# Optimization experiments

Measured on AMD Instinct MI355X. Metric: run time of the kernel, lower is better.

Reference implementation:

```python
import jax, jax.numpy as jnp
import numpy as np
import math

HIDDEN = 1024
HEADS = 16
HEAD_DIM = HIDDEN // HEADS
TEMP_K = 1000.0  # custom temperature multiplier applied after masking
B, S = 2, 2048


def setup_inputs() -> dict:
    key = jax.random.key(0)
    ks = jax.random.split(key, 4)
    scale = 1.0 / math.sqrt(HIDDEN)
    return {
        "x": jax.random.normal(ks[0], (B, S, HIDDEN), dtype=jnp.float32),
        "W_qkv": jax.random.normal(ks[1], (HIDDEN, 3 * HIDDEN), dtype=jnp.float32) * scale,
        "b_qkv": jnp.zeros((3 * HIDDEN,), dtype=jnp.float32),
        "W_out": jax.random.normal(ks[2], (HIDDEN, HIDDEN), dtype=jnp.float32) * scale,
        "b_out": jnp.zeros((HIDDEN,), dtype=jnp.float32),
    }


def reference(x, W_qkv, b_qkv, W_out, b_out):
    b, s, _ = x.shape
    qkv = x @ W_qkv + b_qkv                                    # [b,s,3*hidden]
    qkv = qkv.reshape(b, s, 3, HEADS, HEAD_DIM)
    qkv = jnp.transpose(qkv, (2, 0, 3, 1, 4))                  # [3,b,h,s,d]
    q, k, v = qkv[0], qkv[1], qkv[2]
    scores = jnp.einsum('bhqd,bhkd->bhqk', q, k) / math.sqrt(HEAD_DIM)
    causal = jnp.tril(jnp.ones((s, s), dtype=bool))            # [s,s]
    scores = jnp.where(causal[None, None], scores, -jnp.inf)
    probs = jax.nn.softmax(scores * TEMP_K, axis=-1)           # temp-scaled softmax
    attn = jnp.einsum('bhqk,bhkd->bhqd', probs, v)             # [b,h,s,d]
    attn = jnp.transpose(attn, (0, 2, 1, 3)).reshape(b, s, HIDDEN)
    return attn @ W_out + b_out
```

## Files before the change

### kernel.cpp

```cpp
#include <hip/hip_runtime.h>
#include <hip/hip_bf16.h>

#define BATCH 2
#define SEQ 2048
#define HID 1024
#define NHEAD 16
#define HDIM 64
#define L2SCALE 180.3368800721f
#define NEGBIG (-1.0e30f)

typedef __bf16 bf16;
typedef __bf16 bf16x4 __attribute__((ext_vector_type(4)));
typedef __bf16 bf16x8 __attribute__((ext_vector_type(8)));
typedef float f32x16 __attribute__((ext_vector_type(16)));

union BQ  { bf16x4 v; unsigned u[2]; };
union BF8 { bf16x8 v; unsigned u[4]; };

__device__ __constant__ int TAB_QT[30]  = {5,6,7,8,9,10,11,11,12,12,13,13,14,14,15,15, 4,10, 3,9,15, 2,8,14, 1,7,13, 0,6,12};
__device__ __constant__ int TAB_K0[30]  = {0,0,0,0,0,0,0,12,0,12,0,12,0,12,0,12, 0,12, 0,12,24, 0,12,24, 0,12,24, 0,12,24};
__device__ __constant__ int TAB_NIT[30] = {12,12,12,12,12,12,12,12,12,12,12,12,12,12,12,12, 10,10, 8,8,8, 6,6,6, 4,4,4, 2,2,2};
__device__ __constant__ int TAB_PID[30] = {-1,0,2,4,6,8,10,11,12,13,15,16,18,19,21,22, -1,9, -1,7,23, -1,5,20, -1,3,17, -1,1,14};

__global__ __launch_bounds__(256) void transpose_split_kernel(
    const float* __restrict__ W, bf16* __restrict__ Thi, bf16* __restrict__ Tlo,
    int K, int N)
{
    __shared__ float T[64][65];
    const int tid = threadIdx.x;
    const int kBase = blockIdx.y * 64;
    const int nBase = blockIdx.x * 64;
    {
        const int k0 = tid >> 4;
        const int nc = (tid & 15) * 4;
#pragma unroll
        for (int kk = 0; kk < 4; kk++) {
            int k = k0 + kk * 16;
            float4 v = *(const float4*)(W + (size_t)(kBase + k) * N + nBase + nc);
            T[k][nc] = v.x; T[k][nc + 1] = v.y; T[k][nc + 2] = v.z; T[k][nc + 3] = v.w;
        }
    }
    __syncthreads();
    {
        const int n = tid >> 2;
        const int kc = (tid & 3) * 16;
        bf16x8 h0, h1, l0, l1;
#pragma unroll
        for (int j = 0; j < 8; j++) {
            float a = T[kc + j][n];
            float c = T[kc + 8 + j][n];
            bf16 ha = (bf16)a, hc = (bf16)c;
            h0[j] = ha; h1[j] = hc;
            l0[j] = (bf16)(a - (float)ha);
            l1[j] = (bf16)(c - (float)hc);
        }
        size_t dst = (size_t)(nBase + n) * K + kBase + kc;
        *(bf16x8*)(Thi + dst)     = h0;
        *(bf16x8*)(Thi + dst + 8) = h1;
        if (Tlo) {
            *(bf16x8*)(Tlo + dst)     = l0;
            *(bf16x8*)(Tlo + dst + 8) = l1;
        }
    }
}

__global__ __launch_bounds__(256) void xsplit_kernel(
    const float* __restrict__ X, bf16* __restrict__ Xhi, bf16* __restrict__ Xlo)
{
    const int i = blockIdx.x * 256 + threadIdx.x;
    float4 v = ((const float4*)X)[i];
    float xs[4] = {v.x, v.y, v.z, v.w};
    bf16x4 h, l;
#pragma unroll
    for (int j = 0; j < 4; j++) {
        h[j] = (bf16)xs[j];
        l[j] = (bf16)(xs[j] - (float)h[j]);
    }
    ((bf16x4*)Xhi)[i] = h;
    ((bf16x4*)Xlo)[i] = l;
}

__global__ __launch_bounds__(256) void vtrans_kernel(
    const bf16* __restrict__ vv, bf16* __restrict__ vtr)
{
    __shared__ bf16 T[64][72];
    const int tid = threadIdx.x;
    const int bh = blockIdx.y;
    const int st = blockIdx.x;
    const int r  = tid >> 2;
    const int c0 = (tid & 3) * 16;
    const bf16* src = vv + ((size_t)bh * SEQ + st * 64) * HDIM;
    bf16x8 a = *(const bf16x8*)(src + (size_t)r * HDIM + c0);
    bf16x8 b = *(const bf16x8*)(src + (size_t)r * HDIM + c0 + 8);
    *(bf16x8*)&T[r][c0]     = a;
    *(bf16x8*)&T[r][c0 + 8] = b;
    __syncthreads();
    bf16x8 o0, o1;
#pragma unroll
    for (int i = 0; i < 8; i++) {
        o0[i] = T[c0 + i][r];
        o1[i] = T[c0 + 8 + i][r];
    }
    bf16* dst = vtr + ((size_t)bh * HDIM + r) * SEQ + st * 64 + c0;
    *(bf16x8*)(dst)     = o0;
    *(bf16x8*)(dst + 8) = o1;
}

__global__ __launch_bounds__(256) void gemm_qkv_mfma(
    const bf16* __restrict__ Xhi, const bf16* __restrict__ Xlo,
    const bf16* __restrict__ Wthi, const bf16* __restrict__ Wtlo,
    const float* __restrict__ bias,
    bf16* __restrict__ qhi, bf16* __restrict__ qlo,
    bf16* __restrict__ khi, bf16* __restrict__ klo, bf16* __restrict__ vv)
{
    __shared__ __align__(16) bf16 Wh[128][40];
    __shared__ __align__(16) bf16 Wl[128][40];

    const int tid = threadIdx.x;
    const int wave = tid >> 6, lane = tid & 63;
    const int lm = lane & 31, lq2 = lane >> 5;
    const int wave_s = wave & 1, wave_n = wave >> 1;
    const int nBase = blockIdx.x * 128;
    const int sBase = blockIdx.y * 128;
    const bool isV = (nBase >= 2 * HID);

    const int sr = tid >> 1, skc = (tid & 1) * 16;

    f32x16 acc[2][2];
#pragma unroll
    for (int st = 0; st < 2; st++)
#pragma unroll
      for (int nt = 0; nt < 2; nt++)
#pragma unroll
        for (int r = 0; r < 16; r++) acc[st][nt][r] = 0.f;

    const bf16* xph[2];
    const bf16* xpl[2];
#pragma unroll
    for (int st = 0; st < 2; st++) {
        size_t row = (size_t)(sBase + wave_s * 64 + st * 32 + lm);
        xph[st] = Xhi + row * HID + lq2 * 8;
        xpl[st] = Xlo + row * HID + lq2 * 8;
    }
    const bf16* wbh = Wthi + (size_t)(nBase + sr) * HID + skc;
    const bf16* wbl = Wtlo + (size_t)(nBase + sr) * HID + skc;

    bf16x8 cw[2], cwl[2] = {};
    cw[0] = *(const bf16x8*)(wbh);
    cw[1] = *(const bf16x8*)(wbh + 8);
    if (!isV) {
        cwl[0] = *(const bf16x8*)(wbl);
        cwl[1] = *(const bf16x8*)(wbl + 8);
    }

    for (int k0 = 0; k0 < HID; k0 += 32) {
        bf16x8 xh_c[2][2], xl_c[2][2] = {};
#pragma unroll
        for (int st = 0; st < 2; st++)
#pragma unroll
          for (int kh = 0; kh < 2; kh++) {
            xh_c[st][kh] = *(const bf16x8*)(xph[st] + k0 + kh * 16);
            if (!isV) xl_c[st][kh] = *(const bf16x8*)(xpl[st] + k0 + kh * 16);
          }

        __syncthreads();
        *(bf16x8*)&Wh[sr][skc]     = cw[0];
        *(bf16x8*)&Wh[sr][skc + 8] = cw[1];
        if (!isV) {
            *(bf16x8*)&Wl[sr][skc]     = cwl[0];
            *(bf16x8*)&Wl[sr][skc + 8] = cwl[1];
        }
        __syncthreads();

        bf16x8 nw[2] = {}, nwl[2] = {};
        if (k0 + 32 < HID) {
            nw[0] = *(const bf16x8*)(wbh + k0 + 32);
            nw[1] = *(const bf16x8*)(wbh + k0 + 32 + 8);
            if (!isV) {
                nwl[0] = *(const bf16x8*)(wbl + k0 + 32);
                nwl[1] = *(const bf16x8*)(wbl + k0 + 32 + 8);
            }
        }

#pragma unroll
        for (int kh = 0; kh < 2; kh++) {
            const int ko = kh * 16 + lq2 * 8;
            bf16x8 aWh[2], aWl[2];
#pragma unroll
            for (int nt = 0; nt < 2; nt++) {
                aWh[nt] = *(bf16x8*)&Wh[wave_n * 64 + nt * 32 + lm][ko];
                if (!isV) aWl[nt] = *(bf16x8*)&Wl[wave_n * 64 + nt * 32 + lm][ko];
            }
#pragma unroll
            for (int nt = 0; nt < 2; nt++)
#pragma unroll
              for (int st = 0; st < 2; st++) {
                acc[st][nt] = __builtin_amdgcn_mfma_f32_32x32x16_bf16(aWh[nt], xh_c[st][kh], acc[st][nt], 0, 0, 0);
                if (!isV) {
                    acc[st][nt] = __builtin_amdgcn_mfma_f32_32x32x16_bf16(aWh[nt], xl_c[st][kh], acc[st][nt], 0, 0, 0);
                    acc[st][nt] = __builtin_amdgcn_mfma_f32_32x32x16_bf16(aWl[nt], xh_c[st][kh], acc[st][nt], 0, 0, 0);
                }
              }
        }
        cw[0] = nw[0]; cw[1] = nw[1];
        cwl[0] = nwl[0]; cwl[1] = nwl[1];
    }

#pragma unroll
    for (int st = 0; st < 2; st++) {
        int s = sBase + wave_s * 64 + st * 32 + lm;
        int bb = s >> 11, ss = s & 2047;
#pragma unroll
        for (int nt = 0; nt < 2; nt++) {
#pragma unroll
            for (int q4 = 0; q4 < 4; q4++) {
                int n = nBase + wave_n * 64 + nt * 32 + 8 * q4 + 4 * lq2;
                float4 bv = *(const float4*)(bias + n);
                float vals[4];
                vals[0] = acc[st][nt][q4 * 4 + 0] + bv.x;
                vals[1] = acc[st][nt][q4 * 4 + 1] + bv.y;
                vals[2] = acc[st][nt][q4 * 4 + 2] + bv.z;
                vals[3] = acc[st][nt][q4 * 4 + 3] + bv.w;
                int which = n >> 10, h = (n >> 6) & 15, d = n & 63;
                size_t dst = (((size_t)bb * NHEAD + h) * SEQ + ss) * HDIM + d;
                if (which < 2) {
                    bf16x4 hi4, lo4;
#pragma unroll
                    for (int i = 0; i < 4; i++) {
                        hi4[i] = (bf16)vals[i];
                        lo4[i] = (bf16)(vals[i] - (float)hi4[i]);
                    }
                    bf16* ph = (which == 0) ? qhi : khi;
                    bf16* pl = (which == 0) ? qlo : klo;
                    *(bf16x4*)(ph + dst) = hi4;
                    *(bf16x4*)(pl + dst) = lo4;
                } else {
                    bf16x4 v4;
#pragma unroll
                    for (int i = 0; i < 4; i++) v4[i] = (bf16)vals[i];
                    *(bf16x4*)(vv + dst) = v4;
                }
            }
        }
    }
}

__global__ __launch_bounds__(256) void attn_kernel(
    const bf16* __restrict__ Qhi, const bf16* __restrict__ Qlo,
    const bf16* __restrict__ Khg, const bf16* __restrict__ Klg,
    const bf16* __restrict__ Vtr, bf16* __restrict__ attnbuf,
    bf16* __restrict__ PartO, float* __restrict__ Mls)
{
    __shared__ __align__(16) bf16 Khs[64][72];
    __shared__ __align__(16) bf16 Kls[64][72];
    __shared__ __align__(16) bf16 Vt [64][72];

    const int tid  = threadIdx.x;
    const int wave = tid >> 6;
    const int lane = tid & 63;
    const int lm   = lane & 31;
    const int lq2  = lane >> 5;

    const int kr  = tid >> 2;
    const int kd0 = (tid & 3) * 16;

    const int slot = blockIdx.x >> 5;
    const int bh   = blockIdx.x & 31;
    const int qt   = TAB_QT[slot];
    const int kt0  = TAB_K0[slot];
    const int nit  = TAB_NIT[slot];
    const int pid  = TAB_PID[slot];
    const int b = bh >> 4, h = bh & 15;
    const size_t headoff = ((size_t)b * NHEAD + h) * SEQ * HDIM;

    const int ql_loc = wave * 32 + lm;
    const int qg = qt * 128 + ql_loc;
    bf16x8 qh[4], qlr[4];
    {
        const bf16* qph = Qhi + headoff + (size_t)qg * HDIM;
        const bf16* qpl = Qlo + headoff + (size_t)qg * HDIM;
#pragma unroll
        for (int c = 0; c < 4; c++) {
            qh[c]  = *(const bf16x8*)(qph + c * 16 + lq2 * 8);
            qlr[c] = *(const bf16x8*)(qpl + c * 16 + lq2 * 8);
        }
    }

    f32x16 O0, O1;
#pragma unroll
    for (int r = 0; r < 16; r++) { O0[r] = 0.f; O1[r] = 0.f; }
    float m_run = NEGBIG, l_run = 0.f;

    const int wave_qmin = qt * 128 + wave * 32;
    const int ktend = kt0 + nit;

    bf16x8 kc[4], vc[2];
    {
        size_t kg = headoff + (size_t)(kt0 * 64 + kr) * HDIM + kd0;
        kc[0] = *(const bf16x8*)(Khg + kg);
        kc[1] = *(const bf16x8*)(Khg + kg + 8);
        kc[2] = *(const bf16x8*)(Klg + kg);
        kc[3] = *(const bf16x8*)(Klg + kg + 8);
        size_t vg = headoff + (size_t)kr * SEQ + kt0 * 64 + kd0;
        vc[0] = *(const bf16x8*)(Vtr + vg);
        vc[1] = *(const bf16x8*)(Vtr + vg + 8);
    }

    for (int kt = kt0; kt < ktend; kt++) {
        __syncthreads();
        *(bf16x8*)&Khs[kr][kd0]     = kc[0];
        *(bf16x8*)&Khs[kr][kd0 + 8] = kc[1];
        *(bf16x8*)&Kls[kr][kd0]     = kc[2];
        *(bf16x8*)&Kls[kr][kd0 + 8] = kc[3];
        *(bf16x8*)&Vt[kr][kd0]      = vc[0];
        *(bf16x8*)&Vt[kr][kd0 + 8]  = vc[1];
        __syncthreads();

        bf16x8 kn[4], vn[2];
        const bool more = (kt + 1 < ktend);
        if (more) {
            size_t kg = headoff + (size_t)((kt + 1) * 64 + kr) * HDIM + kd0;
            kn[0] = *(const bf16x8*)(Khg + kg);
            kn[1] = *(const bf16x8*)(Khg + kg + 8);
            kn[2] = *(const bf16x8*)(Klg + kg);
            kn[3] = *(const bf16x8*)(Klg + kg + 8);
            size_t vg = headoff + (size_t)kr * SEQ + (kt + 1) * 64 + kd0;
            vn[0] = *(const bf16x8*)(Vtr + vg);
            vn[1] = *(const bf16x8*)(Vtr + vg + 8);
        }

        if (kt * 64 <= wave_qmin + 31) {
            f32x16 s[2];
#pragma unroll
            for (int r = 0; r < 16; r++) { s[0][r] = 0.f; s[1][r] = 0.f; }
#pragma unroll
            for (int c = 0; c < 4; c++) {
                bf16x8 ah0 = *(bf16x8*)&Khs[lm][c * 16 + lq2 * 8];
                bf16x8 al0 = *(bf16x8*)&Kls[lm][c * 16 + lq2 * 8];
                bf16x8 ah1 = *(bf16x8*)&Khs[32 + lm][c * 16 + lq2 * 8];
                bf16x8 al1 = *(bf16x8*)&Kls[32 + lm][c * 16 + lq2 * 8];
                s[0] = __builtin_amdgcn_mfma_f32_32x32x16_bf16(ah0, qh[c],  s[0], 0, 0, 0);
                s[0] = __builtin_amdgcn_mfma_f32_32x32x16_bf16(ah0, qlr[c], s[0], 0, 0, 0);
                s[0] = __builtin_amdgcn_mfma_f32_32x32x16_bf16(al0, qh[c],  s[0], 0, 0, 0);
                s[1] = __builtin_amdgcn_mfma_f32_32x32x16_bf16(ah1, qh[c],  s[1], 0, 0, 0);
                s[1] = __builtin_amdgcn_mfma_f32_32x32x16_bf16(ah1, qlr[c], s[1], 0, 0, 0);
                s[1] = __builtin_amdgcn_mfma_f32_32x32x16_bf16(al1, qh[c],  s[1], 0, 0, 0);
            }

            if (kt * 64 + 63 > wave_qmin) {
                const int kbase = kt * 64 + 4 * lq2;
#pragma unroll
                for (int mt = 0; mt < 2; mt++)
#pragma unroll
                  for (int r = 0; r < 16; r++) {
                    int koff = (r & 3) + 8 * (r >> 2) + 32 * mt;
                    float L = s[mt][r] * L2SCALE;
                    if (kbase + koff > qg) L = NEGBIG;
                    s[mt][r] = L;
                  }
            } else {
#pragma unroll
                for (int mt = 0; mt < 2; mt++)
#pragma unroll
                  for (int r = 0; r < 16; r++) s[mt][r] *= L2SCALE;
            }

            float vmax = NEGBIG;
#pragma unroll
            for (int r = 0; r < 16; r++)
                vmax = fmaxf(vmax, fmaxf(s[0][r], s[1][r]));
            vmax = fmaxf(vmax, __shfl_xor(vmax, 32, 64));
            float mnew = fmaxf(m_run, vmax);
            float alpha = exp2f(m_run - mnew);
            float sum = 0.f;
#pragma unroll
            for (int mt = 0; mt < 2; mt++)
#pragma unroll
              for (int r = 0; r < 16; r++) {
                s[mt][r] = exp2f(s[mt][r] - mnew);
                sum += s[mt][r];
              }
            sum += __shfl_xor(sum, 32, 64);
            l_run = l_run * alpha + sum;
            m_run = mnew;
#pragma unroll
            for (int r = 0; r < 16; r++) { O0[r] *= alpha; O1[r] *= alpha; }

            bf16x8 pfrag[4];
#pragma unroll
            for (int mt = 0; mt < 2; mt++)
#pragma unroll
              for (int hh = 0; hh < 2; hh++) {
                BQ A, B;
#pragma unroll
                for (int i = 0; i < 4; i++) {
                    A.v[i] = (bf16)s[mt][8 * hh + i];
                    B.v[i] = (bf16)s[mt][8 * hh + 4 + i];
                }
                unsigned s0_ = lq2 ? A.u[0] : B.u[0];
                unsigned s1_ = lq2 ? A.u[1] : B.u[1];
                unsigned r0 = __shfl_xor(s0_, 32, 64);
                unsigned r1 = __shfl_xor(s1_, 32, 64);
                BF8 f;
                f.u[0] = lq2 ? r0 : A.u[0];
                f.u[1] = lq2 ? r1 : A.u[1];
                f.u[2] = lq2 ? B.u[0] : r0;
                f.u[3] = lq2 ? B.u[1] : r1;
                pfrag[mt * 2 + hh] = f.v;
              }

#pragma unroll
            for (int c = 0; c < 4; c++) {
                bf16x8 va0 = *(bf16x8*)&Vt[lm][c * 16 + lq2 * 8];
                bf16x8 va1 = *(bf16x8*)&Vt[32 + lm][c * 16 + lq2 * 8];
                O0 = __builtin_amdgcn_mfma_f32_32x32x16_bf16(va0, pfrag[c], O0, 0, 0, 0);
                O1 = __builtin_amdgcn_mfma_f32_32x32x16_bf16(va1, pfrag[c], O1, 0, 0, 0);
            }
        }

        if (more) {
#pragma unroll
            for (int i = 0; i < 4; i++) kc[i] = kn[i];
            vc[0] = vn[0]; vc[1] = vn[1];
        }
    }

    if (pid < 0) {
        const float inv = 1.0f / l_run;
        bf16* orow = attnbuf + ((size_t)b * SEQ + qg) * HID + h * HDIM;
#pragma unroll
        for (int g = 0; g < 4; g++) {
            int d0 = 8 * g + 4 * lq2;
            bf16x4 o0, o1;
#pragma unroll
            for (int i = 0; i < 4; i++) {
                o0[i] = (bf16)(O0[4 * g + i] * inv);
                o1[i] = (bf16)(O1[4 * g + i] * inv);
            }
            *(bf16x4*)(orow + d0)      = o0;
            *(bf16x4*)(orow + 32 + d0) = o1;
        }
    } else {
        bf16* prow = PartO + (((size_t)pid * 32 + bh) * 128 + ql_loc) * HDIM;
#pragma unroll
        for (int g = 0; g < 4; g++) {
            int d0 = 8 * g + 4 * lq2;
            bf16x4 o0, o1;
#pragma unroll
            for (int i = 0; i < 4; i++) {
                o0[i] = (bf16)O0[4 * g + i];
                o1[i] = (bf16)O1[4 * g + i];
            }
            *(bf16x4*)(prow + d0)      = o0;
            *(bf16x4*)(prow + 32 + d0) = o1;
        }
        if (lq2 == 0) {
            float2 ml = make_float2(m_run, l_run);
            *(float2*)&Mls[(((size_t)pid * 32 + bh) * 128 + ql_loc) * 2] = ml;
        }
    }
}

__global__ __launch_bounds__(256) void attn_combine(
    const bf16* __restrict__ PartO, const float* __restrict__ Mls,
    bf16* __restrict__ attnbuf)
{
    const int tid = threadIdx.x;
    const int qt = 6 + blockIdx.x / 32;
    const int bh = blockIdx.x & 31;
    const int b = bh >> 4, h = bh & 15;
    const int qrow = tid >> 1;
    const int dh = (tid & 1) * 32;

    int pid0, nch;
    if (qt < 12) { pid0 = 2 * (qt - 6); nch = 2; }
    else         { pid0 = 12 + 3 * (qt - 12); nch = 3; }

    float mv[3], lv[3];
    float M = NEGBIG;
#pragma unroll
    for (int c = 0; c < 3; c++) {
        if (c < nch) {
            float2 ml = *(const float2*)&Mls[(((size_t)(pid0 + c) * 32 + bh) * 128 + qrow) * 2];
            mv[c] = ml.x; lv[c] = ml.y;
            M = fmaxf(M, mv[c]);
        }
    }
    float L = 0.f;
    float acc[32];
#pragma unroll
    for (int i = 0; i < 32; i++) acc[i] = 0.f;
#pragma unroll
    for (int c = 0; c < 3; c++) {
        if (c < nch) {
            float w = exp2f(mv[c] - M);
            L += w * lv[c];
            const bf16* p = PartO + (((size_t)(pid0 + c) * 32 + bh) * 128 + qrow) * HDIM + dh;
#pragma unroll
            for (int g = 0; g < 4; g++) {
                bf16x8 v = *(const bf16x8*)(p + g * 8);
#pragma unroll
                for (int i = 0; i < 8; i++) acc[g * 8 + i] += w * (float)v[i];
            }
        }
    }
    const float inv = 1.0f / L;
    bf16* orow = attnbuf + ((size_t)b * SEQ + qt * 128 + qrow) * HID + h * HDIM + dh;
#pragma unroll
    for (int g = 0; g < 4; g++) {
        bf16x8 o;
#pragma unroll
        for (int i = 0; i < 8; i++) o[i] = (bf16)(acc[g * 8 + i] * inv);
        *(bf16x8*)(orow + g * 8) = o;
    }
}

__global__ __launch_bounds__(256) void gemm_out_mfma(
    const bf16* __restrict__ Attn, const bf16* __restrict__ Wt,
    const float* __restrict__ bias, float* __restrict__ out)
{
    __shared__ __align__(16) bf16 Ah[64][40];

    const int tid = threadIdx.x;
    const int wave = tid >> 6, lane = tid & 63;
    const int lm = lane & 31, lq2 = lane >> 5;
    const int nBase = blockIdx.x * 64;
    const int mBase = blockIdx.y * 128;

    const int ar = tid >> 2, akc = (tid & 3) * 8;
    const bf16* bp    = Attn + (size_t)(mBase + wave * 32 + lm) * HID + lq2 * 8;
    const bf16* abase = Wt + (size_t)(nBase + ar) * HID + akc;

    f32x16 acc[2];
#pragma unroll
    for (int nt = 0; nt < 2; nt++)
#pragma unroll
      for (int r = 0; r < 16; r++) acc[nt][r] = 0.f;

    bf16x8 ca = *(const bf16x8*)(abase);

    for (int k0 = 0; k0 < HID; k0 += 32) {
        bf16x8 cb[2];
        cb[0] = *(const bf16x8*)(bp + k0);
        cb[1] = *(const bf16x8*)(bp + k0 + 16);

        __syncthreads();
        *(bf16x8*)&Ah[ar][akc] = ca;
        __syncthreads();

        bf16x8 na = {};
        if (k0 + 32 < HID) na = *(const bf16x8*)(abase + k0 + 32);

#pragma unroll
        for (int kh = 0; kh < 2; kh++) {
            const int ko = kh * 16 + lq2 * 8;
            bf16x8 aW0 = *(bf16x8*)&Ah[lm][ko];
            bf16x8 aW1 = *(bf16x8*)&Ah[32 + lm][ko];
            acc[0] = __builtin_amdgcn_mfma_f32_32x32x16_bf16(aW0, cb[kh], acc[0], 0, 0, 0);
            acc[1] = __builtin_amdgcn_mfma_f32_32x32x16_bf16(aW1, cb[kh], acc[1], 0, 0, 0);
        }
        ca = na;
    }

    const int m = mBase + wave * 32 + lm;
#pragma unroll
    for (int nt = 0; nt < 2; nt++) {
#pragma unroll
        for (int q4 = 0; q4 < 4; q4++) {
            int n = nBase + nt * 32 + 8 * q4 + 4 * lq2;
            float4 bv = *(const float4*)(bias + n);
            float4 o;
            o.x = acc[nt][q4 * 4 + 0] + bv.x;
            o.y = acc[nt][q4 * 4 + 1] + bv.y;
            o.z = acc[nt][q4 * 4 + 2] + bv.z;
            o.w = acc[nt][q4 * 4 + 3] + bv.w;
            *(float4*)(out + (size_t)m * HID + n) = o;
        }
    }
}

extern "C" void kernel_launch(void* const* d_in, const int* in_sizes, int n_in,
                              void* d_out, int out_size, void* d_ws, size_t ws_size,
                              hipStream_t stream) {
    const float* x    = (const float*)d_in[0];
    const float* Wqkv = (const float*)d_in[1];
    const float* bqkv = (const float*)d_in[2];
    const float* Wout = (const float*)d_in[3];
    const float* bout = (const float*)d_in[4];
    float* out = (float*)d_out;

    const size_t NW  = (size_t)HID * 3 * HID;
    const size_t NWo = (size_t)HID * HID;
    const size_t NT  = (size_t)BATCH * NHEAD * SEQ * HDIM;
    bf16* Wthi = (bf16*)d_ws;
    bf16* Wtlo = Wthi + NW;
    bf16* Wot  = Wtlo + NW;
    bf16* qhi  = Wot + NWo;
    bf16* qlo  = qhi + NT;
    bf16* khi  = qlo + NT;
    bf16* klo  = khi + NT;
    bf16* vv   = klo + NT;
    bf16* attnbuf = vv + NT;
    bf16* Xhi  = attnbuf;
    bf16* Xlo  = attnbuf + NT;
    bf16* vtr  = Xlo;
    bf16* PartO = Wthi;
    float* Mls  = (float*)vv;

    xsplit_kernel<<<dim3((BATCH * SEQ * HID) / 1024), 256, 0, stream>>>(x, Xhi, Xlo);
    transpose_split_kernel<<<dim3(3 * HID / 64, HID / 64), 256, 0, stream>>>(
        Wqkv, Wthi, Wtlo, HID, 3 * HID);
    transpose_split_kernel<<<dim3(HID / 64, HID / 64), 256, 0, stream>>>(
        Wout, Wot, nullptr, HID, HID);
    gemm_qkv_mfma<<<dim3(3 * HID / 128, BATCH * SEQ / 128), 256, 0, stream>>>(
        Xhi, Xlo, Wthi, Wtlo, bqkv, qhi, qlo, khi, klo, vv);
    vtrans_kernel<<<dim3(SEQ / 64, BATCH * NHEAD), 256, 0, stream>>>(vv, vtr);
    attn_kernel<<<dim3(960), 256, 0, stream>>>(
        qhi, qlo, khi, klo, vtr, attnbuf, PartO, Mls);
    attn_combine<<<dim3(320), 256, 0, stream>>>(PartO, Mls, attnbuf);
    gemm_out_mfma<<<dim3(HID / 64, BATCH * SEQ / 128), 256, 0, stream>>>(
        attnbuf, Wot, bout, out);
}
```

Measured before the change: 293.7 us.

## Merge prep kernels, prefetch X tiles in QKV GEMM, enlarge output GEMM tile

Folds the x split and both weight transpose/split kernels into a single prep launch dispatched by block index, which saves two kernel launches. The QKV GEMM now register-prefetches the next X fragments one k-step ahead and changes its shared-memory weight staging layout. The output projection GEMM moves from a 64-wide to a 128x128 tile with a 2x2 wave layout, raising MFMA work per shared-memory load. The cost is higher register pressure and half as many output-GEMM blocks, which may reduce occupancy.

New measurement: 332.0 us. +13.1%, slower.

```diff
diff --git a/kernel.cpp b/kernel.cpp
--- a/kernel.cpp
+++ b/kernel.cpp
@@ -22,14 +22,10 @@
 __device__ __constant__ int TAB_NIT[30] = {12,12,12,12,12,12,12,12,12,12,12,12,12,12,12,12, 10,10, 8,8,8, 6,6,6, 4,4,4, 2,2,2};
 __device__ __constant__ int TAB_PID[30] = {-1,0,2,4,6,8,10,11,12,13,15,16,18,19,21,22, -1,9, -1,7,23, -1,5,20, -1,3,17, -1,1,14};
 
-__global__ __launch_bounds__(256) void transpose_split_kernel(
-    const float* __restrict__ W, bf16* __restrict__ Thi, bf16* __restrict__ Tlo,
-    int K, int N)
+__device__ __forceinline__ void transpose_split_body(
+    float (*T)[65], const float* __restrict__ W, bf16* __restrict__ Thi,
+    bf16* __restrict__ Tlo, int K, int N, int kBase, int nBase, int tid)
 {
-    __shared__ float T[64][65];
-    const int tid = threadIdx.x;
-    const int kBase = blockIdx.y * 64;
-    const int nBase = blockIdx.x * 64;
     {
         const int k0 = tid >> 4;
         const int nc = (tid & 15) * 4;
@@ -64,20 +60,35 @@
     }
 }
 
-__global__ __launch_bounds__(256) void xsplit_kernel(
-    const float* __restrict__ X, bf16* __restrict__ Xhi, bf16* __restrict__ Xlo)
+__global__ __launch_bounds__(256) void prep_kernel(
+    const float* __restrict__ X, bf16* __restrict__ Xhi, bf16* __restrict__ Xlo,
+    const float* __restrict__ Wqkv, bf16* __restrict__ Wthi, bf16* __restrict__ Wtlo,
+    const float* __restrict__ Wout, bf16* __restrict__ Wot)
 {
-    const int i = blockIdx.x * 256 + threadIdx.x;
-    float4 v = ((const float4*)X)[i];
-    float xs[4] = {v.x, v.y, v.z, v.w};
-    bf16x4 h, l;
-#pragma unroll
-    for (int j = 0; j < 4; j++) {
-        h[j] = (bf16)xs[j];
-        l[j] = (bf16)(xs[j] - (float)h[j]);
-    }
-    ((bf16x4*)Xhi)[i] = h;
-    ((bf16x4*)Xlo)[i] = l;
+    __shared__ float T[64][65];
+    const int tid = threadIdx.x;
+    const int bid = blockIdx.x;
+    if (bid < 4096) {
+        const int i = bid * 256 + tid;
+        float4 v = ((const float4*)X)[i];
+        float xs[4] = {v.x, v.y, v.z, v.w};
+        bf16x4 h, l;
+#pragma unroll
+        for (int j = 0; j < 4; j++) {
+            h[j] = (bf16)xs[j];
+            l[j] = (bf16)(xs[j] - (float)h[j]);
+        }
+        ((bf16x4*)Xhi)[i] = h;
+        ((bf16x4*)Xlo)[i] = l;
+    } else if (bid < 4096 + 768) {
+        const int r = bid - 4096;
+        transpose_split_body(T, Wqkv, Wthi, Wtlo, HID, 3 * HID,
+                             (r / 48) * 64, (r % 48) * 64, tid);
+    } else {
+        const int r = bid - 4864;
+        transpose_split_body(T, Wout, Wot, nullptr, HID, HID,
+                             (r / 16) * 64, (r % 16) * 64, tid);
+    }
 }
 
 __global__ __launch_bounds__(256) void vtrans_kernel(
@@ -113,8 +124,8 @@
     bf16* __restrict__ qhi, bf16* __restrict__ qlo,
     bf16* __restrict__ khi, bf16* __restrict__ klo, bf16* __restrict__ vv)
 {
-    __shared__ __align__(16) bf16 Wh[128][40];
-    __shared__ __align__(16) bf16 Wl[128][40];
+    __shared__ __align__(16) bf16 Wh[128][72];
+    __shared__ __align__(16) bf16 Wl[128][72];
 
     const int tid = threadIdx.x;
     const int wave = tid >> 6, lane = tid & 63;
@@ -124,7 +135,8 @@
     const int sBase = blockIdx.y * 128;
     const bool isV = (nBase >= 2 * HID);
 
-    const int sr = tid >> 1, skc = (tid & 1) * 16;
+    const int wr = tid >> 2;
+    const int wc = (tid & 3) * 8;
 
     f32x16 acc[2][2];
 #pragma unroll
@@ -142,43 +154,56 @@
         xph[st] = Xhi + row * HID + lq2 * 8;
         xpl[st] = Xlo + row * HID + lq2 * 8;
     }
-    const bf16* wbh = Wthi + (size_t)(nBase + sr) * HID + skc;
-    const bf16* wbl = Wtlo + (size_t)(nBase + sr) * HID + skc;
+    const bf16* wbh0 = Wthi + (size_t)(nBase + wr) * HID + wc;
+    const bf16* wbh1 = Wthi + (size_t)(nBase + 64 + wr) * HID + wc;
+    const bf16* wbl0 = Wtlo + (size_t)(nBase + wr) * HID + wc;
+    const bf16* wbl1 = Wtlo + (size_t)(nBase + 64 + wr) * HID + wc;
 
     bf16x8 cw[2], cwl[2] = {};
-    cw[0] = *(const bf16x8*)(wbh);
-    cw[1] = *(const bf16x8*)(wbh + 8);
+    cw[0] = *(const bf16x8*)(wbh0);
+    cw[1] = *(const bf16x8*)(wbh1);
     if (!isV) {
-        cwl[0] = *(const bf16x8*)(wbl);
-        cwl[1] = *(const bf16x8*)(wbl + 8);
-    }
+        cwl[0] = *(const bf16x8*)(wbl0);
+        cwl[1] = *(const bf16x8*)(wbl1);
+    }
+    bf16x8 xc[2][2], xcl[2][2] = {};
+#pragma unroll
+    for (int st = 0; st < 2; st++)
+#pragma unroll
+      for (int kh = 0; kh < 2; kh++) {
+        xc[st][kh] = *(const bf16x8*)(xph[st] + kh * 16);
+        if (!isV) xcl[st][kh] = *(const bf16x8*)(xpl[st] + kh * 16);
+      }
 
     for (int k0 = 0; k0 < HID; k0 += 32) {
-        bf16x8 xh_c[2][2], xl_c[2][2] = {};
-#pragma unroll
-        for (int st = 0; st < 2; st++)
-#pragma unroll
-          for (int kh = 0; kh < 2; kh++) {
-            xh_c[st][kh] = *(const bf16x8*)(xph[st] + k0 + kh * 16);
-            if (!isV) xl_c[st][kh] = *(const bf16x8*)(xpl[st] + k0 + kh * 16);
-          }
+        const bool more = (k0 + 32 < HID);
+        bf16x8 xn[2][2] = {}, xnl[2][2] = {};
+        if (more) {
+#pragma unroll
+            for (int st = 0; st < 2; st++)
+#pragma unroll
+              for (int kh = 0; kh < 2; kh++) {
+                xn[st][kh] = *(const bf16x8*)(xph[st] + k0 + 32 + kh * 16);
+                if (!isV) xnl[st][kh] = *(const bf16x8*)(xpl[st] + k0 + 32 + kh * 16);
+              }
+        }
 
         __syncthreads();
-        *(bf16x8*)&Wh[sr][skc]     = cw[0];
-        *(bf16x8*)&Wh[sr][skc + 8] = cw[1];
+        *(bf16x8*)&Wh[wr][wc]      = cw[0];
+        *(bf16x8*)&Wh[64 + wr][wc] = cw[1];
         if (!isV) {
-            *(bf16x8*)&Wl[sr][skc]     = cwl[0];
-            *(bf16x8*)&Wl[sr][skc + 8] = cwl[1];
+            *(bf16x8*)&Wl[wr][wc]      = cwl[0];
+            *(bf16x8*)&Wl[64 + wr][wc] = cwl[1];
         }
         __syncthreads();
 
         bf16x8 nw[2] = {}, nwl[2] = {};
-        if (k0 + 32 < HID) {
-            nw[0] = *(const bf16x8*)(wbh + k0 + 32);
-            nw[1] = *(const bf16x8*)(wbh + k0 + 32 + 8);
+        if (more) {
+            nw[0] = *(const bf16x8*)(wbh0 + k0 + 32);
+            nw[1] = *(const bf16x8*)(wbh1 + k0 + 32);
             if (!isV) {
-                nwl[0] = *(const bf16x8*)(wbl + k0 + 32);
-                nwl[1] = *(const bf16x8*)(wbl + k0 + 32 + 8);
+                nwl[0] = *(const bf16x8*)(wbl0 + k0 + 32);
+                nwl[1] = *(const bf16x8*)(wbl1 + k0 + 32);
             }
         }
 
@@ -195,13 +220,20 @@
             for (int nt = 0; nt < 2; nt++)
 #pragma unroll
               for (int st = 0; st < 2; st++) {
-                acc[st][nt] = __builtin_amdgcn_mfma_f32_32x32x16_bf16(aWh[nt], xh_c[st][kh], acc[st][nt], 0, 0, 0);
+                acc[st][nt] = __builtin_amdgcn_mfma_f32_32x32x16_bf16(aWh[nt], xc[st][kh], acc[st][nt], 0, 0, 0);
                 if (!isV) {
-                    acc[st][nt] = __builtin_amdgcn_mfma_f32_32x32x16_bf16(aWh[nt], xl_c[st][kh], acc[st][nt], 0, 0, 0);
-                    acc[st][nt] = __builtin_amdgcn_mfma_f32_32x32x16_bf16(aWl[nt], xh_c[st][kh], acc[st][nt], 0, 0, 0);
+                    acc[st][nt] = __builtin_amdgcn_mfma_f32_32x32x16_bf16(aWh[nt], xcl[st][kh], acc[st][nt], 0, 0, 0);
+                    acc[st][nt] = __builtin_amdgcn_mfma_f32_32x32x16_bf16(aWl[nt], xc[st][kh], acc[st][nt], 0, 0, 0);
                 }
               }
         }
+#pragma unroll
+        for (int st = 0; st < 2; st++)
+#pragma unroll
+          for (int kh = 0; kh < 2; kh++) {
+            xc[st][kh] = xn[st][kh];
+            xcl[st][kh] = xnl[st][kh];
+          }
         cw[0] = nw[0]; cw[1] = nw[1];
         cwl[0] = nwl[0]; cwl[1] = nwl[1];
     }
@@ -519,62 +551,101 @@
     const bf16* __restrict__ Attn, const bf16* __restrict__ Wt,
     const float* __restrict__ bias, float* __restrict__ out)
 {
-    __shared__ __align__(16) bf16 Ah[64][40];
+    __shared__ __align__(16) bf16 Ah[128][72];
 
     const int tid = threadIdx.x;
     const int wave = tid >> 6, lane = tid & 63;
     const int lm = lane & 31, lq2 = lane >> 5;
-    const int nBase = blockIdx.x * 64;
+    const int wave_m = wave & 1, wave_n = wave >> 1;
+    const int nBase = blockIdx.x * 128;
     const int mBase = blockIdx.y * 128;
 
-    const int ar = tid >> 2, akc = (tid & 3) * 8;
-    const bf16* bp    = Attn + (size_t)(mBase + wave * 32 + lm) * HID + lq2 * 8;
-    const bf16* abase = Wt + (size_t)(nBase + ar) * HID + akc;
-
-    f32x16 acc[2];
-#pragma unroll
-    for (int nt = 0; nt < 2; nt++)
-#pragma unroll
-      for (int r = 0; r < 16; r++) acc[nt][r] = 0.f;
-
-    bf16x8 ca = *(const bf16x8*)(abase);
+    const int wr = tid >> 2;
+    const int wc = (tid & 3) * 8;
+    const bf16* ab0 = Wt + (size_t)(nBase + wr) * HID + wc;
+    const bf16* ab1 = Wt + (size_t)(nBase + 64 + wr) * HID + wc;
+
+    const bf16* bp[2];
+#pragma unroll
+    for (int st = 0; st < 2; st++)
+        bp[st] = Attn + (size_t)(mBase + wave_m * 64 + st * 32 + lm) * HID + lq2 * 8;
+
+    f32x16 acc[2][2];
+#pragma unroll
+    for (int st = 0; st < 2; st++)
+#pragma unroll
+      for (int nt = 0; nt < 2; nt++)
+#pragma unroll
+        for (int r = 0; r < 16; r++) acc[st][nt][r] = 0.f;
+
+    bf16x8 ca[2];
+    ca[0] = *(const bf16x8*)(ab0);
+    ca[1] = *(const bf16x8*)(ab1);
+    bf16x8 cb[2][2];
+#pragma unroll
+    for (int st = 0; st < 2; st++)
+#pragma unroll
+      for (int kh = 0; kh < 2; kh++)
+        cb[st][kh] = *(const bf16x8*)(bp[st] + kh * 16);
 
     for (int k0 = 0; k0 < HID; k0 += 32) {
-        bf16x8 cb[2];
-        cb[0] = *(const bf16x8*)(bp + k0);
-        cb[1] = *(const bf16x8*)(bp + k0 + 16);
+        const bool more = (k0 + 32 < HID);
+        bf16x8 nb[2][2] = {};
+        if (more) {
+#pragma unroll
+            for (int st = 0; st < 2; st++)
+#pragma unroll
+              for (int kh = 0; kh < 2; kh++)
+                nb[st][kh] = *(const bf16x8*)(bp[st] + k0 + 32 + kh * 16);
+        }
 
         __syncthreads();
-        *(bf16x8*)&Ah[ar][akc] = ca;
+        *(bf16x8*)&Ah[wr][wc]      = ca[0];
+        *(bf16x8*)&Ah[64 + wr][wc] = ca[1];
         __syncthreads();
 
-        bf16x8 na = {};
-        if (k0 + 32 < HID) na = *(const bf16x8*)(abase + k0 + 32);
+        bf16x8 na[2] = {};
+        if (more) {
+            na[0] = *(const bf16x8*)(ab0 + k0 + 32);
+            na[1] = *(const bf16x8*)(ab1 + k0 + 32);
+        }
 
 #pragma unroll
         for (int kh = 0; kh < 2; kh++) {
             const int ko = kh * 16 + lq2 * 8;
-            bf16x8 aW0 = *(bf16x8*)&Ah[lm][ko];
-            bf16x8 aW1 = *(bf16x8*)&Ah[32 + lm][ko];
-            acc[0] = __builtin_amdgcn_mfma_f32_32x32x16_bf16(aW0, cb[kh], acc[0], 0, 0, 0);
-            acc[1] = __builtin_amdgcn_mfma_f32_32x32x16_bf16(aW1, cb[kh], acc[1], 0, 0, 0);
-        }
-        ca = na;
-    }
-
-    const int m = mBase + wave * 32 + lm;
-#pragma unroll
-    for (int nt = 0; nt < 2; nt++) {
-#pragma unroll
-        for (int q4 = 0; q4 < 4; q4++) {
-            int n = nBase + nt * 32 + 8 * q4 + 4 * lq2;
-            float4 bv = *(const float4*)(bias + n);
-            float4 o;
-            o.x = acc[nt][q4 * 4 + 0] + bv.x;
-            o.y = acc[nt][q4 * 4 + 1] + bv.y;
-            o.z = acc[nt][q4 * 4 + 2] + bv.z;
-            o.w = acc[nt][q4 * 4 + 3] + bv.w;
-            *(float4*)(out + (size_t)m * HID + n) = o;
+            bf16x8 aW[2];
+#pragma unroll
+            for (int nt = 0; nt < 2; nt++)
+                aW[nt] = *(bf16x8*)&Ah[wave_n * 64 + nt * 32 + lm][ko];
+#pragma unroll
+            for (int nt = 0; nt < 2; nt++)
+#pragma unroll
+              for (int st = 0; st < 2; st++)
+                acc[st][nt] = __builtin_amdgcn_mfma_f32_32x32x16_bf16(aW[nt], cb[st][kh], acc[st][nt], 0, 0, 0);
+        }
+#pragma unroll
+        for (int st = 0; st < 2; st++)
+#pragma unroll
+          for (int kh = 0; kh < 2; kh++) cb[st][kh] = nb[st][kh];
+        ca[0] = na[0]; ca[1] = na[1];
+    }
+
+#pragma unroll
+    for (int st = 0; st < 2; st++) {
+        int m = mBase + wave_m * 64 + st * 32 + lm;
+#pragma unroll
+        for (int nt = 0; nt < 2; nt++) {
+#pragma unroll
+            for (int q4 = 0; q4 < 4; q4++) {
+                int n = nBase + wave_n * 64 + nt * 32 + 8 * q4 + 4 * lq2;
+                float4 bv = *(const float4*)(bias + n);
+                float4 o;
+                o.x = acc[st][nt][q4 * 4 + 0] + bv.x;
+                o.y = acc[st][nt][q4 * 4 + 1] + bv.y;
+                o.z = acc[st][nt][q4 * 4 + 2] + bv.z;
+                o.w = acc[st][nt][q4 * 4 + 3] + bv.w;
+                *(float4*)(out + (size_t)m * HID + n) = o;
+            }
         }
     }
 }
@@ -607,17 +678,14 @@
     bf16* PartO = Wthi;
     float* Mls  = (float*)vv;
 
-    xsplit_kernel<<<dim3((BATCH * SEQ * HID) / 1024), 256, 0, stream>>>(x, Xhi, Xlo);
-    transpose_split_kernel<<<dim3(3 * HID / 64, HID / 64), 256, 0, stream>>>(
-        Wqkv, Wthi, Wtlo, HID, 3 * HID);
-    transpose_split_kernel<<<dim3(HID / 64, HID / 64), 256, 0, stream>>>(
-        Wout, Wot, nullptr, HID, HID);
+    prep_kernel<<<dim3(4096 + 768 + 256), 256, 0, stream>>>(
+        x, Xhi, Xlo, Wqkv, Wthi, Wtlo, Wout, Wot);
     gemm_qkv_mfma<<<dim3(3 * HID / 128, BATCH * SEQ / 128), 256, 0, stream>>>(
         Xhi, Xlo, Wthi, Wtlo, bqkv, qhi, qlo, khi, klo, vv);
     vtrans_kernel<<<dim3(SEQ / 64, BATCH * NHEAD), 256, 0, stream>>>(vv, vtr);
     attn_kernel<<<dim3(960), 256, 0, stream>>>(
         qhi, qlo, khi, klo, vtr, attnbuf, PartO, Mls);
     attn_combine<<<dim3(320), 256, 0, stream>>>(PartO, Mls, attnbuf);
-    gemm_out_mfma<<<dim3(HID / 64, BATCH * SEQ / 128), 256, 0, stream>>>(
+    gemm_out_mfma<<<dim3(HID / 128, BATCH * SEQ / 128), 256, 0, stream>>>(
         attnbuf, Wot, bout, out);
 }
```
